# Kernel tuning notes

Measured on AMD Instinct MI355X. Metric: run time of the kernel, lower is better.

Reference implementation:

```python
import jax, jax.numpy as jnp
import numpy as np

B, L, D_MODEL, N_HEADS = 4, 2048, 1024, 16
HEAD_DIM = D_MODEL // N_HEADS


def setup_inputs() -> dict:
    key = jax.random.key(0)
    ks = jax.random.split(key, 11)
    s = 1.0 / np.sqrt(D_MODEL)
    return {
        "queries": jax.random.normal(ks[0], (B, L, D_MODEL), jnp.float32),
        "keys": jax.random.normal(ks[1], (B, L, D_MODEL), jnp.float32),
        "values": jax.random.normal(ks[2], (B, L, D_MODEL), jnp.float32),
        "Wq": jax.random.normal(ks[3], (D_MODEL, D_MODEL), jnp.float32) * s,
        "bq": jnp.zeros((D_MODEL,), jnp.float32),
        "Wk": jax.random.normal(ks[4], (D_MODEL, D_MODEL), jnp.float32) * s,
        "bk": jnp.zeros((D_MODEL,), jnp.float32),
        "Wv": jax.random.normal(ks[5], (D_MODEL, D_MODEL), jnp.float32) * s,
        "bv": jnp.zeros((D_MODEL,), jnp.float32),
        "Wo": jax.random.normal(ks[6], (D_MODEL, D_MODEL), jnp.float32) * s,
        "bo": jnp.zeros((D_MODEL,), jnp.float32),
    }


def reference(queries, keys, values, Wq, bq, Wk, bk, Wv, bv, Wo, bo):
    Bsz, Lq, _ = queries.shape
    S = keys.shape[1]
    H, E = N_HEADS, HEAD_DIM
    # QKV projections (weights stored [in, out])
    q = (queries @ Wq + bq).reshape(Bsz, Lq, H, E)
    k = (keys @ Wk + bk).reshape(Bsz, S, H, E)
    v = (values @ Wv + bv).reshape(Bsz, S, H, E)
    scale = 1.0 / np.sqrt(E)
    # scores: [B, H, L, S]
    scores = jnp.einsum("blhe,bshe->bhls", q, k)
    A = jax.nn.softmax(scale * scores, axis=-1)
    # context: [B, L, H, E] -> [B, L, D]
    ctx = jnp.einsum("bhls,bshd->blhd", A, v).reshape(Bsz, Lq, H * E)
    out = ctx @ Wo + bo
    return out
```

## Files before the change

### kernel.cpp

```cpp
#include <hip/hip_runtime.h>

#define BATCH 4
#define SEQ   2048
#define DMODEL 1024
#define NHEADS 16
#define HDIM  64
#define MROWS (BATCH * SEQ)

typedef float f32x4 __attribute__((ext_vector_type(4)));
typedef short s16x8 __attribute__((ext_vector_type(8)));
typedef short s16x4 __attribute__((ext_vector_type(4)));
typedef unsigned short u16;

#define MFMA32K(a, b, c) __builtin_amdgcn_mfma_f32_16x16x32_bf16((a), (b), (c), 0, 0, 0)
#define MFMA16K(a, b, c) __builtin_amdgcn_mfma_f32_16x16x16bf16_1k((a), (b), (c), 0, 0, 0)

__device__ __forceinline__ u16 f2bf(float x) {
    unsigned int u = __builtin_bit_cast(unsigned int, x);
    unsigned int r = u + 0x7fffu + ((u >> 16) & 1u);
    return (u16)(r >> 16);
}

#if __has_builtin(__builtin_amdgcn_cvt_pk_bf16_f32)
__device__ __forceinline__ unsigned int pack2bf(float a, float b) {
    auto r = __builtin_amdgcn_cvt_pk_bf16_f32(a, b);
    return __builtin_bit_cast(unsigned int, r);
}
#else
__device__ __forceinline__ unsigned int pack2bf(float a, float b) {
    return (unsigned int)f2bf(a) | ((unsigned int)f2bf(b) << 16);
}
#endif

__device__ __forceinline__ void dma16(const u16* g, const u16* l) {
    __builtin_amdgcn_global_load_lds(
        (const __attribute__((address_space(1))) unsigned int*)g,
        (__attribute__((address_space(3))) unsigned int*)l, 16, 0, 0);
}

__global__ __launch_bounds__(256) void prep(
    const float* __restrict__ s0, const float* __restrict__ s1,
    const float* __restrict__ s2, u16* __restrict__ d0, u16* __restrict__ d1,
    u16* __restrict__ d2, const float* __restrict__ W0,
    const float* __restrict__ W1, const float* __restrict__ W2,
    const float* __restrict__ W3, u16* __restrict__ Wt) {
    __shared__ u16 tile[64][80];
    const int bid = blockIdx.x;
    const int t = threadIdx.x;
    if (bid < 12288) {
        const int z = bid >> 12, xi = bid & 4095;
        const float* src = (z == 0) ? s0 : (z == 1) ? s1 : s2;
        u16* dst = (z == 0) ? d0 : (z == 1) ? d1 : d2;
        const int i = xi * 256 + t;
        float4 a = ((const float4*)src)[i * 2];
        float4 b = ((const float4*)src)[i * 2 + 1];
        uint4 o;
        o.x = pack2bf(a.x, a.y); o.y = pack2bf(a.z, a.w);
        o.z = pack2bf(b.x, b.y); o.w = pack2bf(b.z, b.w);
        *(uint4*)(dst + (size_t)i * 8) = o;
    } else {
        const int wb = bid - 12288;
        const int mtx = wb >> 8;
        const int rem = wb & 255;
        const float* W = (mtx == 0) ? W0 : (mtx == 1) ? W1 : (mtx == 2) ? W2 : W3;
        u16* out = Wt + (size_t)mtx * DMODEL * DMODEL;
        const int n0 = (rem & 15) * 64, k0 = (rem >> 4) * 64;
#pragma unroll
        for (int j = 0; j < 4; ++j) {
            int k = j * 16 + (t >> 4);
            int c = (t & 15) * 4;
            float4 v = *(const float4*)(W + (size_t)(k0 + k) * DMODEL + n0 + c);
            tile[c + 0][k] = f2bf(v.x);
            tile[c + 1][k] = f2bf(v.y);
            tile[c + 2][k] = f2bf(v.z);
            tile[c + 3][k] = f2bf(v.w);
        }
        __syncthreads();
#pragma unroll
        for (int i2 = 0; i2 < 2; ++i2) {
            int n = i2 * 32 + (t >> 3), ck = (t & 7) * 8;
            uint4 v = *(const uint4*)(&tile[n][ck]);
            *(uint4*)(out + (size_t)(n0 + n) * DMODEL + k0 + ck) = v;
        }
    }
}

__global__ __launch_bounds__(256) void gemm_qkv(
    const u16* __restrict__ Aq, const u16* __restrict__ Ak,
    const u16* __restrict__ Av, const u16* __restrict__ Wt,
    const float* __restrict__ biq, const float* __restrict__ bik,
    const float* __restrict__ biv, u16* __restrict__ oq, u16* __restrict__ ok,
    u16* __restrict__ ov, float sq) {
    __shared__ u16 As0[128 * 32];
    __shared__ u16 Bs0[128 * 32];
    __shared__ u16 As1[128 * 32];
    __shared__ u16 Bs1[128 * 32];
    const int t = threadIdx.x;
    const int w = t >> 6, lane = t & 63, quad = lane >> 4, l16 = lane & 15;
    const int z = blockIdx.z;
    const u16* A = (z == 0) ? Aq : (z == 1) ? Ak : Av;
    const u16* B = Wt + (size_t)z * DMODEL * DMODEL;
    const float* bias = (z == 0) ? biq : (z == 1) ? bik : biv;
    u16* C = (z == 0) ? oq : (z == 1) ? ok : ov;
    const float scale = (z == 0) ? sq : 1.0f;
    const int m0 = blockIdx.x * 128, n0 = blockIdx.y * 128;
    const int wm = (w >> 1) * 64, wn = (w & 1) * 64;

    const int srow = lane >> 2;
    const int sunit = (lane & 3) ^ (srow & 3);
    const u16* aBase = A + (size_t)(m0 + w * 32 + srow) * DMODEL + sunit * 8;
    const u16* bBase = B + (size_t)(n0 + w * 32 + srow) * DMODEL + sunit * 8;
    const int un8 = (quad ^ (l16 & 3)) * 8;

    f32x4 acc[4][4] = {};

#define STAGE(AS_, BS_, kt_)                                                   \
    do {                                                                       \
        dma16(aBase + (kt_) * 32,                &AS_[(w * 32) * 32]);         \
        dma16(aBase + 16 * DMODEL + (kt_) * 32,  &AS_[(w * 32 + 16) * 32]);    \
        dma16(bBase + (kt_) * 32,                &BS_[(w * 32) * 32]);         \
        dma16(bBase + 16 * DMODEL + (kt_) * 32,  &BS_[(w * 32 + 16) * 32]);    \
    } while (0)

#define WAITC4 asm volatile("s_waitcnt vmcnt(4)" ::: "memory")
#define WAITC0 asm volatile("s_waitcnt vmcnt(0)" ::: "memory")
#define BAR()                                                                  \
    do {                                                                       \
        asm volatile("s_barrier" ::: "memory");                                \
        __builtin_amdgcn_sched_barrier(0);                                     \
    } while (0)

#define COMPUTE(AS_, BS_)                                                      \
    do {                                                                       \
        s16x8 af[4], bf[4];                                                    \
        _Pragma("unroll")                                                      \
        for (int mt = 0; mt < 4; ++mt) {                                       \
            af[mt] = *(const s16x8*)(&AS_[(wm + mt * 16 + l16) * 32 + un8]);   \
            bf[mt] = *(const s16x8*)(&BS_[(wn + mt * 16 + l16) * 32 + un8]);   \
        }                                                                      \
        _Pragma("unroll")                                                      \
        for (int mt = 0; mt < 4; ++mt) {                                       \
            _Pragma("unroll")                                                  \
            for (int nt = 0; nt < 4; ++nt)                                     \
                acc[mt][nt] = MFMA32K(af[mt], bf[nt], acc[mt][nt]);            \
        }                                                                      \
    } while (0)

    const int NT = DMODEL / 32;
    STAGE(As0, Bs0, 0);
    for (int tt = 0; tt < NT - 2; tt += 2) {
        STAGE(As1, Bs1, tt + 1);
        WAITC4; BAR();
        COMPUTE(As0, Bs0);
        BAR();
        STAGE(As0, Bs0, tt + 2);
        WAITC4; BAR();
        COMPUTE(As1, Bs1);
        BAR();
    }
    STAGE(As1, Bs1, NT - 1);
    WAITC4; BAR();
    COMPUTE(As0, Bs0);
    BAR();
    WAITC0; BAR();
    COMPUTE(As1, Bs1);

#undef STAGE
#undef WAITC4
#undef WAITC0
#undef BAR
#undef COMPUTE

#pragma unroll
    for (int mt = 0; mt < 4; ++mt)
#pragma unroll
        for (int nt = 0; nt < 4; ++nt) {
            int col = n0 + wn + nt * 16 + l16;
            float bv_ = bias[col];
#pragma unroll
            for (int r = 0; r < 4; ++r) {
                int row = m0 + wm + mt * 16 + quad * 4 + r;
                C[(size_t)row * DMODEL + col] = f2bf((acc[mt][nt][r] + bv_) * scale);
            }
        }
}

__global__ __launch_bounds__(256) void gemm_o(const u16* __restrict__ A,
                                              const u16* __restrict__ Bt,
                                              const float* __restrict__ bias,
                                              float* __restrict__ Cp) {
    __shared__ u16 As[128 * 64];
    __shared__ u16 Bs[128 * 64];
    const int t = threadIdx.x;
    const int w = t >> 6, lane = t & 63, quad = lane >> 4, l16 = lane & 15;
    const int m0 = blockIdx.x * 128, n0 = blockIdx.y * 128;
    const int wm = (w >> 1) * 64, wn = (w & 1) * 64;
    const int lr8 = lane >> 3;
    const int lun = (lane & 7) ^ lr8;

    f32x4 acc[4][4] = {};

    for (int k0 = 0; k0 < DMODEL; k0 += 64) {
#pragma unroll
        for (int j = 0; j < 4; ++j) {
            int r8 = w * 32 + j * 8;
            dma16(A + (size_t)(m0 + r8 + lr8) * DMODEL + k0 + lun * 8, &As[r8 * 64]);
            dma16(Bt + (size_t)(n0 + r8 + lr8) * DMODEL + k0 + lun * 8, &Bs[r8 * 64]);
        }
        __syncthreads();
#pragma unroll
        for (int half = 0; half < 2; ++half) {
            s16x8 af[4], bf[4];
#pragma unroll
            for (int mt = 0; mt < 4; ++mt) {
                int un = ((half * 4 + quad) ^ (l16 & 7)) * 8;
                af[mt] = *(const s16x8*)(&As[(wm + mt * 16 + l16) * 64 + un]);
                bf[mt] = *(const s16x8*)(&Bs[(wn + mt * 16 + l16) * 64 + un]);
            }
#pragma unroll
            for (int mt = 0; mt < 4; ++mt)
#pragma unroll
                for (int nt = 0; nt < 4; ++nt)
                    acc[mt][nt] = MFMA32K(af[mt], bf[nt], acc[mt][nt]);
        }
        __syncthreads();
    }

#pragma unroll
    for (int mt = 0; mt < 4; ++mt)
#pragma unroll
        for (int nt = 0; nt < 4; ++nt) {
            int col = n0 + wn + nt * 16 + l16;
            float bv_ = bias[col];
#pragma unroll
            for (int r = 0; r < 4; ++r) {
                int row = m0 + wm + mt * 16 + quad * 4 + r;
                Cp[(size_t)row * DMODEL + col] = acc[mt][nt][r] + bv_;
            }
        }
}

__global__ __launch_bounds__(256, 2) void attn3(const u16* __restrict__ qb,
                                                const u16* __restrict__ kb,
                                                const u16* __restrict__ vb,
                                                u16* __restrict__ ctxb) {
    __shared__ u16 Ks[64 * 64];
    __shared__ u16 Vt[80 * 72];
    const int t = threadIdx.x;
    const int w = t >> 6, lane = t & 63, quad = lane >> 4, l16 = lane & 15;
    const int h = blockIdx.x, b = blockIdx.z, q0 = blockIdx.y * 256;

    s16x8 bq[4][2];
#pragma unroll
    for (int qs = 0; qs < 4; ++qs) {
        size_t base = (size_t)(b * SEQ + q0 + w * 64 + qs * 16 + l16) * DMODEL + h * HDIM + quad * 8;
        bq[qs][0] = *(const s16x8*)(qb + base);
        bq[qs][1] = *(const s16x8*)(qb + base + 32);
    }

    for (int idx = t; idx < 16 * 72; idx += 256) {
        int r = idx / 72, c = idx - r * 72;
        Vt[(64 + r) * 72 + c] = (r == 0) ? (u16)0x3F80 : (u16)0;
    }

    const int krow = lane >> 3;
    const int kunit = (lane & 7) ^ (krow & 7);

    f32x4 o[4][5] = {};

    for (int s0 = 0; s0 < SEQ; s0 += 64) {
        __syncthreads();
#pragma unroll
        for (int j = 0; j < 2; ++j) {
            int row = w * 16 + j * 8 + krow;
            dma16(kb + (size_t)(b * SEQ + s0 + row) * DMODEL + h * HDIM + kunit * 8,
                  &Ks[(w * 16 + j * 8) * 64]);
        }
#pragma unroll
        for (int i = 0; i < 2; ++i) {
            int idx = i * 256 + t;
            int key = idx >> 3, seg = idx & 7;
            union { uint4 v; u16 s[8]; } u;
            u.v = *(const uint4*)(vb + (size_t)(b * SEQ + s0 + key) * DMODEL + h * HDIM + seg * 8);
            int col = (((key >> 3) ^ seg) << 3) + (key & 7);
#pragma unroll
            for (int ii = 0; ii < 8; ++ii)
                Vt[(seg * 8 + ii) * 72 + col] = u.s[ii];
        }
        __syncthreads();

        s16x8 ak[4][2];
#pragma unroll
        for (int kt = 0; kt < 4; ++kt) {
            int row = kt * 16 + l16;
#pragma unroll
            for (int hf = 0; hf < 2; ++hf) {
                int un = (hf * 4 + quad) ^ (l16 & 7);
                ak[kt][hf] = *(const s16x8*)(&Ks[row * 64 + un * 8]);
            }
        }

        unsigned int pk[4][4][2];
#pragma unroll
        for (int qs = 0; qs < 4; ++qs) {
            f32x4 sc[4];
#pragma unroll
            for (int kt = 0; kt < 4; ++kt) {
                f32x4 zz = {0.0f, 0.0f, 0.0f, 0.0f};
                zz = MFMA32K(ak[kt][0], bq[qs][0], zz);
                sc[kt] = MFMA32K(ak[kt][1], bq[qs][1], zz);
            }
#pragma unroll
            for (int kt = 0; kt < 4; ++kt) {
                float p0 = __builtin_amdgcn_exp2f(sc[kt][0]);
                float p1 = __builtin_amdgcn_exp2f(sc[kt][1]);
                float p2 = __builtin_amdgcn_exp2f(sc[kt][2]);
                float p3 = __builtin_amdgcn_exp2f(sc[kt][3]);
                pk[qs][kt][0] = pack2bf(p0, p1);
                pk[qs][kt][1] = pack2bf(p2, p3);
            }
        }

#pragma unroll
        for (int mt = 0; mt < 5; ++mt) {
            const int dim = mt * 16 + l16;
            const int swz = (dim >> 3) & 7;
            const int rowoff = dim * 72;
#pragma unroll
            for (int kt = 0; kt < 4; ++kt) {
                int col = ((((kt * 2) + (quad >> 1)) ^ swz) << 3) + ((quad & 1) << 2);
                s16x4 av = *(const s16x4*)(&Vt[rowoff + col]);
#pragma unroll
                for (int qs = 0; qs < 4; ++qs) {
                    union { unsigned int u[2]; s16x4 v; } pb;
                    pb.u[0] = pk[qs][kt][0];
                    pb.u[1] = pk[qs][kt][1];
                    o[qs][mt] = MFMA16K(av, pb.v, o[qs][mt]);
                }
            }
        }
    }

#pragma unroll
    for (int qs = 0; qs < 4; ++qs) {
        float ls = __shfl(o[qs][4][0], l16);
        float rl = 1.0f / ls;
        size_t rowbase = (size_t)(b * SEQ + q0 + w * 64 + qs * 16 + l16) * DMODEL + h * HDIM;
#pragma unroll
        for (int mt = 0; mt < 4; ++mt)
#pragma unroll
            for (int rr = 0; rr < 2; ++rr) {
                unsigned int v = pack2bf(o[qs][mt][rr * 2] * rl, o[qs][mt][rr * 2 + 1] * rl);
                *(unsigned int*)(&ctxb[rowbase + mt * 16 + quad * 4 + rr * 2]) = v;
            }
    }
}

extern "C" void kernel_launch(void* const* d_in, const int* in_sizes, int n_in,
                              void* d_out, int out_size, void* d_ws, size_t ws_size,
                              hipStream_t stream) {
    const float* queries = (const float*)d_in[0];
    const float* keys    = (const float*)d_in[1];
    const float* values  = (const float*)d_in[2];
    const float* Wq = (const float*)d_in[3];
    const float* bq = (const float*)d_in[4];
    const float* Wk = (const float*)d_in[5];
    const float* bk = (const float*)d_in[6];
    const float* Wv = (const float*)d_in[7];
    const float* bv = (const float*)d_in[8];
    const float* Wo = (const float*)d_in[9];
    const float* bo = (const float*)d_in[10];
    float* out = (float*)d_out;

    char* ws = (char*)d_ws;
    u16* Wt   = (u16*)ws;
    u16* aq   = (u16*)(ws + ((size_t)8 << 20));
    u16* ak   = (u16*)(ws + ((size_t)24 << 20));
    u16* av   = (u16*)(ws + ((size_t)40 << 20));
    u16* qbuf = (u16*)(ws + ((size_t)56 << 20));
    u16* kbuf = (u16*)(ws + ((size_t)72 << 20));
    u16* vbuf = (u16*)(ws + ((size_t)88 << 20));
    u16* ctxb = qbuf;

    const size_t WSZ = (size_t)DMODEL * DMODEL;
    const float S2 = 0.125f * 1.44269504088896340736f;

    dim3 blk(256);

    prep<<<dim3(13312), blk, 0, stream>>>(queries, keys, values, aq, ak, av,
                                          Wq, Wk, Wv, Wo, Wt);

    gemm_qkv<<<dim3(64, 8, 3), blk, 0, stream>>>(aq, ak, av, Wt,
                                                 bq, bk, bv, qbuf, kbuf, vbuf, S2);

    attn3<<<dim3(NHEADS, SEQ / 256, BATCH), blk, 0, stream>>>(qbuf, kbuf, vbuf, ctxb);

    gemm_o<<<dim3(64, 8), blk, 0, stream>>>(ctxb, Wt + 3 * WSZ, bo, out);
}
```

Baseline: 342.7 us.

## Double-buffer output projection GEMM with async DMA prefetch and K=32 stages

```diff
diff --git a/kernel.cpp b/kernel.cpp
--- a/kernel.cpp
+++ b/kernel.cpp
@@ -189,42 +189,79 @@
                                               const u16* __restrict__ Bt,
                                               const float* __restrict__ bias,
                                               float* __restrict__ Cp) {
-    __shared__ u16 As[128 * 64];
-    __shared__ u16 Bs[128 * 64];
+    __shared__ u16 As0[128 * 32];
+    __shared__ u16 Bs0[128 * 32];
+    __shared__ u16 As1[128 * 32];
+    __shared__ u16 Bs1[128 * 32];
     const int t = threadIdx.x;
     const int w = t >> 6, lane = t & 63, quad = lane >> 4, l16 = lane & 15;
     const int m0 = blockIdx.x * 128, n0 = blockIdx.y * 128;
     const int wm = (w >> 1) * 64, wn = (w & 1) * 64;
-    const int lr8 = lane >> 3;
-    const int lun = (lane & 7) ^ lr8;
+
+    const int srow = lane >> 2;
+    const int sunit = (lane & 3) ^ (srow & 3);
+    const u16* aBase = A + (size_t)(m0 + w * 32 + srow) * DMODEL + sunit * 8;
+    const u16* bBase = Bt + (size_t)(n0 + w * 32 + srow) * DMODEL + sunit * 8;
+    const int un8 = (quad ^ (l16 & 3)) * 8;
 
     f32x4 acc[4][4] = {};
 
-    for (int k0 = 0; k0 < DMODEL; k0 += 64) {
-#pragma unroll
-        for (int j = 0; j < 4; ++j) {
-            int r8 = w * 32 + j * 8;
-            dma16(A + (size_t)(m0 + r8 + lr8) * DMODEL + k0 + lun * 8, &As[r8 * 64]);
-            dma16(Bt + (size_t)(n0 + r8 + lr8) * DMODEL + k0 + lun * 8, &Bs[r8 * 64]);
-        }
-        __syncthreads();
-#pragma unroll
-        for (int half = 0; half < 2; ++half) {
-            s16x8 af[4], bf[4];
-#pragma unroll
-            for (int mt = 0; mt < 4; ++mt) {
-                int un = ((half * 4 + quad) ^ (l16 & 7)) * 8;
-                af[mt] = *(const s16x8*)(&As[(wm + mt * 16 + l16) * 64 + un]);
-                bf[mt] = *(const s16x8*)(&Bs[(wn + mt * 16 + l16) * 64 + un]);
-            }
-#pragma unroll
-            for (int mt = 0; mt < 4; ++mt)
-#pragma unroll
-                for (int nt = 0; nt < 4; ++nt)
-                    acc[mt][nt] = MFMA32K(af[mt], bf[nt], acc[mt][nt]);
-        }
-        __syncthreads();
-    }
+#define STAGE(AS_, BS_, kt_)                                                   \
+    do {                                                                       \
+        dma16(aBase + (kt_) * 32,                &AS_[(w * 32) * 32]);         \
+        dma16(aBase + 16 * DMODEL + (kt_) * 32,  &AS_[(w * 32 + 16) * 32]);    \
+        dma16(bBase + (kt_) * 32,                &BS_[(w * 32) * 32]);         \
+        dma16(bBase + 16 * DMODEL + (kt_) * 32,  &BS_[(w * 32 + 16) * 32]);    \
+    } while (0)
+
+#define WAITC4 asm volatile("s_waitcnt vmcnt(4)" ::: "memory")
+#define WAITC0 asm volatile("s_waitcnt vmcnt(0)" ::: "memory")
+#define BAR()                                                                  \
+    do {                                                                       \
+        asm volatile("s_barrier" ::: "memory");                                \
+        __builtin_amdgcn_sched_barrier(0);                                     \
+    } while (0)
+
+#define COMPUTE(AS_, BS_)                                                      \
+    do {                                                                       \
+        s16x8 af[4], bf[4];                                                    \
+        _Pragma("unroll")                                                      \
+        for (int mt = 0; mt < 4; ++mt) {                                       \
+            af[mt] = *(const s16x8*)(&AS_[(wm + mt * 16 + l16) * 32 + un8]);   \
+            bf[mt] = *(const s16x8*)(&BS_[(wn + mt * 16 + l16) * 32 + un8]);   \
+        }                                                                      \
+        _Pragma("unroll")                                                      \
+        for (int mt = 0; mt < 4; ++mt) {                                       \
+            _Pragma("unroll")                                                  \
+            for (int nt = 0; nt < 4; ++nt)                                     \
+                acc[mt][nt] = MFMA32K(af[mt], bf[nt], acc[mt][nt]);            \
+        }                                                                      \
+    } while (0)
+
+    const int NT = DMODEL / 32;
+    STAGE(As0, Bs0, 0);
+    for (int tt = 0; tt < NT - 2; tt += 2) {
+        STAGE(As1, Bs1, tt + 1);
+        WAITC4; BAR();
+        COMPUTE(As0, Bs0);
+        BAR();
+        STAGE(As0, Bs0, tt + 2);
+        WAITC4; BAR();
+        COMPUTE(As1, Bs1);
+        BAR();
+    }
+    STAGE(As1, Bs1, NT - 1);
+    WAITC4; BAR();
+    COMPUTE(As0, Bs0);
+    BAR();
+    WAITC0; BAR();
+    COMPUTE(As1, Bs1);
+
+#undef STAGE
+#undef WAITC4
+#undef WAITC0
+#undef BAR
+#undef COMPUTE
 
 #pragma unroll
     for (int mt = 0; mt < 4; ++mt)
```

New measurement: 357.8 us. +4.4%, slower.
